# Kernel optimization log

Measured on AMD Instinct MI355X. Metric: run time of the kernel, lower is better.

Reference implementation:

```python
import jax, jax.numpy as jnp
import numpy as np

N = 100000
E = 800000
NFEAT = 128
NHID = 128
NCLASS = 40
THRESHOLD = 0.1
EPS = 1e-8


def setup_inputs() -> dict:
    key = jax.random.key(0)
    ks = jax.random.split(key, 12)
    x = jax.random.normal(ks[0], (N, NFEAT), dtype=jnp.float32)
    edge_index = jax.random.randint(ks[1], (2, E), 0, N, dtype=jnp.int64)
    edge_index2 = jax.random.randint(ks[2], (2, E), 0, N, dtype=jnp.int64)
    s1 = 1.0 / np.sqrt(NFEAT)
    s2 = 1.0 / np.sqrt(NHID)
    s3 = 1.0 / np.sqrt(NCLASS)
    W_gc1 = jax.random.uniform(ks[3], (NFEAT, NHID), jnp.float32, -s1, s1)
    b_gc1 = jax.random.uniform(ks[4], (NHID,), jnp.float32, -s1, s1)
    W_gc2 = jax.random.uniform(ks[5], (NHID, NCLASS), jnp.float32, -s2, s2)
    b_gc2 = jax.random.uniform(ks[6], (NCLASS,), jnp.float32, -s2, s2)
    W_att1 = jax.random.uniform(ks[7], (NCLASS, NCLASS), jnp.float32, -s3, s3)
    b_att1 = jax.random.uniform(ks[8], (NCLASS,), jnp.float32, -s3, s3)
    W_att2 = jax.random.uniform(ks[9], (NCLASS, 1), jnp.float32, -s3, s3)
    return {"x": x, "W_gc1": W_gc1, "b_gc1": b_gc1, "W_gc2": W_gc2,
            "b_gc2": b_gc2, "W_att1": W_att1, "b_att1": b_att1,
            "W_att2": W_att2, "edge_index": edge_index, "edge_index2": edge_index2}


def att_coef(feat, row, col, alive):
    # cosine similarity per edge; edges failing the threshold get weight 0
    # (exactly equivalent to removing them: contribute 0 to degree & messages).
    a = feat[row]          # [E, d]
    b = feat[col]          # [E, d]
    dot = jnp.sum(a * b, axis=-1)
    na = jnp.maximum(jnp.linalg.norm(a, axis=-1), EPS)
    nb = jnp.maximum(jnp.linalg.norm(b, axis=-1), EPS)
    sims = dot / (na * nb)
    mask = alive & (sims >= THRESHOLD)
    # original computes this under torch.no_grad()
    ew = jax.lax.stop_gradient(jnp.where(mask, sims, 0.0))
    return ew, mask


def gcn_conv(x, row, col, ew, W, b):
    # PyG GCNConv with add_self_loops=True, normalize=True on weighted adjacency
    h = x @ W                                     # [N, out]
    deg = jax.ops.segment_sum(ew, row, num_segments=N) + 1.0  # +1 self loop
    dinv = deg ** -0.5
    nw = dinv[row] * ew * dinv[col]               # [E]
    agg = jax.ops.segment_sum(h[col] * nw[:, None], row, num_segments=N)
    agg = agg + h * (dinv * dinv)[:, None]        # self-loop contribution
    return agg + b


def reference(x, W_gc1, b_gc1, W_gc2, b_gc2, W_att1, b_att1, W_att2,
              edge_index, edge_index2):
    r1, c1 = edge_index[0], edge_index[1]
    r2, c2 = edge_index2[0], edge_index2[1]
    ones = jnp.ones((E,), dtype=bool)

    ew2, m2 = att_coef(x, r2, c2, ones)
    ew1, m1 = att_coef(x, r1, c1, ones)

    x2 = jax.nn.relu(gcn_conv(x, r2, c2, ew2, W_gc1, b_gc1))
    x1 = jax.nn.relu(gcn_conv(x, r1, c1, ew1, W_gc1, b_gc1))
    # dropout is identity at eval time

    ew2b, _ = att_coef(x2, r2, c2, m2)
    ew1b, _ = att_coef(x1, r1, c1, m1)

    x2 = gcn_conv(x2, r2, c2, ew2b, W_gc2, b_gc2)
    x1 = gcn_conv(x1, r1, c1, ew1b, W_gc2, b_gc2)

    z = jnp.stack([x1, x2], axis=1)               # [N, 2, C]
    w = jnp.tanh(z @ W_att1 + b_att1) @ W_att2    # [N, 2, 1]
    beta = jax.nn.softmax(w, axis=1)
    fused = jnp.sum(beta * z, axis=1)             # [N, C]
    return jax.nn.log_softmax(fused, axis=1)
```

## Files before the change

### kernel.cpp

```cpp
#include <hip/hip_runtime.h>
#include <hip/hip_bf16.h>

#define NN 100000
#define EE 800000
#define THRV 0.1f
#define DELTA 0.008f
#define EPSV 1e-8f

#define ATOMIC_ADD_F32 unsafeAtomicAdd

__device__ inline int dot4(int a, int b, int c) {
#if __has_builtin(__builtin_amdgcn_sdot4)
    return __builtin_amdgcn_sdot4(a, b, c, false);
#else
    int s = c;
    #pragma unroll
    for (int k = 0; k < 4; k++) {
        int av = (a << (24 - 8 * k)) >> 24;
        int bv = (b << (24 - 8 * k)) >> 24;
        s += av * bv;
    }
    return s;
#endif
}


__global__ __launch_bounds__(256) void normalize_k(const float* __restrict__ x,
                                                   unsigned short* __restrict__ xq,
                                                   float* __restrict__ rs,
                                                   float* __restrict__ norms_x,
                                                   float* __restrict__ degL1) {
    int node = blockIdx.x * 4 + (threadIdx.x >> 6);
    int lane = threadIdx.x & 63;
    float2 v = reinterpret_cast<const float2*>(x)[(size_t)node * 64 + lane];
    float ss = v.x * v.x + v.y * v.y;
    float am = fmaxf(fabsf(v.x), fabsf(v.y));
    #pragma unroll
    for (int off = 32; off; off >>= 1) {
        ss += __shfl_xor(ss, off);
        am = fmaxf(am, __shfl_xor(am, off));
    }
    float norm = fmaxf(sqrtf(ss), EPSV);
    am = fmaxf(am, 1e-12f);
    float qs = 127.0f / am;
    int q0 = __float2int_rn(v.x * qs);
    int q1 = __float2int_rn(v.y * qs);
    unsigned short packed = (unsigned short)((q0 & 0xff) | ((q1 & 0xff) << 8));
    xq[(size_t)node * 64 + lane] = packed;
    if (lane == 0) {
        norms_x[node] = norm;
        rs[node] = am / (127.0f * norm);
        degL1[node] = 1.0f;
        degL1[node + NN] = 1.0f;
    }
}


__global__ __launch_bounds__(256) void edge_sim1_k(
        const unsigned short* __restrict__ xq, const float* __restrict__ rs,
        const float* __restrict__ x, const float* __restrict__ norms_x,
        const int* __restrict__ r1, const int* __restrict__ c1,
        const int* __restrict__ r2, const int* __restrict__ c2,
        float* __restrict__ ews, float* __restrict__ degL1,
        int* __restrict__ cnt) {
    int tid = threadIdx.x;
    int e = blockIdx.x * 16 + (tid >> 4);
    int l16 = tid & 15;
    int rnode, cnode, gr;
    if (e < EE) { rnode = r1[e]; cnode = c1[e]; gr = rnode; }
    else { int ee = e - EE; rnode = r2[ee]; cnode = c2[ee]; gr = NN + rnode; }
    int role = l16 >> 3;
    int j = l16 & 7;
    int node = role ? cnode : rnode;
    uint4 v = reinterpret_cast<const uint4*>(xq)[(size_t)node * 8 + j];
    uint4 p;
    p.x = (unsigned)__shfl_xor((int)v.x, 8);
    p.y = (unsigned)__shfl_xor((int)v.y, 8);
    p.z = (unsigned)__shfl_xor((int)v.z, 8);
    p.w = (unsigned)__shfl_xor((int)v.w, 8);
    int d = dot4((int)v.x, (int)p.x, 0);
    d = dot4((int)v.y, (int)p.y, d);
    d = dot4((int)v.z, (int)p.z, d);
    d = dot4((int)v.w, (int)p.w, d);
    #pragma unroll
    for (int off = 1; off < 8; off <<= 1) d += __shfl_xor(d, off);
    float sim = (float)d * rs[rnode] * rs[cnode];
    if (fabsf(sim - THRV) <= DELTA) {
        const float4* xa = reinterpret_cast<const float4*>(x + (size_t)rnode * 128);
        const float4* xb = reinterpret_cast<const float4*>(x + (size_t)cnode * 128);
        float df = 0.f;
        #pragma unroll
        for (int q = 0; q < 2; q++) {
            float4 a = xa[l16 + 16 * q];
            float4 b = xb[l16 + 16 * q];
            df += a.x * b.x + a.y * b.y + a.z * b.z + a.w * b.w;
        }
        #pragma unroll
        for (int off = 1; off < 16; off <<= 1) df += __shfl_xor(df, off);
        sim = df / (norms_x[rnode] * norms_x[cnode]);
    }
    float w = (sim >= THRV) ? sim : 0.0f;
    if (l16 == 0) {
        ews[e] = w;
        if (w != 0.0f) {
            ATOMIC_ADD_F32(&degL1[gr], w);
            atomicAdd(&cnt[gr], 1);
        }
    }
}


__global__ __launch_bounds__(512) void scan1_k(const int* __restrict__ in,
                                               int* __restrict__ out,
                                               int* __restrict__ partials, int n) {
    __shared__ int a[1024], b[1024];
    int t = threadIdx.x;
    int base = blockIdx.x * 1024;
    a[t]       = (base + t       < n) ? in[base + t]       : 0;
    a[t + 512] = (base + t + 512 < n) ? in[base + t + 512] : 0;
    __syncthreads();
    int* src = a; int* dst = b;
    for (int off = 1; off < 1024; off <<= 1) {
        #pragma unroll
        for (int q = 0; q < 2; q++) {
            int i = t + q * 512;
            int v = src[i];
            if (i >= off) v += src[i - off];
            dst[i] = v;
        }
        __syncthreads();
        int* tmp = src; src = dst; dst = tmp;
    }
    for (int q = 0; q < 2; q++) {
        int i = t + q * 512;
        if (base + i < n) out[base + i] = i ? src[i - 1] : 0;
    }
    if (t == 0) partials[blockIdx.x] = src[1023];
}

__global__ __launch_bounds__(256) void scan2_k(int* __restrict__ partials, int m) {
    __shared__ int a[256], b[256];
    int t = threadIdx.x;
    a[t] = (t < m) ? partials[t] : 0;
    __syncthreads();
    int* src = a; int* dst = b;
    for (int off = 1; off < 256; off <<= 1) {
        int v = src[t];
        if (t >= off) v += src[t - off];
        dst[t] = v;
        __syncthreads();
        int* tmp = src; src = dst; dst = tmp;
    }
    if (t < m) partials[t] = t ? src[t - 1] : 0;
}

__global__ void scan3_k(int* __restrict__ start, int* __restrict__ next,
                        const int* __restrict__ partials,
                        const int* __restrict__ cnt, int n) {
    int i = blockIdx.x * 256 + threadIdx.x;
    if (i < n) {
        int v = start[i] + partials[i >> 10];
        start[i] = v;
        next[i] = v;
        if (i == n - 1) start[n] = v + cnt[i];
    }
}


__global__ void scatter_alive_k(const int* __restrict__ r1, const int* __restrict__ c1,
                                const int* __restrict__ r2, const int* __restrict__ c2,
                                const float* __restrict__ ews,
                                const float* __restrict__ degL1,
                                int* __restrict__ next, int2* __restrict__ acw) {
    int e = blockIdx.x * 256 + threadIdx.x;
    float w = ews[e];
    if (w == 0.0f) return;
    int gr, c, sb;
    if (e < EE) { gr = r1[e]; c = c1[e]; sb = 0; }
    else        { gr = NN + r2[e - EE]; c = c2[e - EE]; sb = NN; }
    int pos = atomicAdd(&next[gr], 1);
    int2 rec;
    rec.x = c;
    rec.y = __float_as_int(w * rsqrtf(degL1[sb + c]));
    acw[pos] = rec;
}


__global__ __launch_bounds__(256) void gemm_nh_k(const float* __restrict__ A,
                                                 const float* __restrict__ W,
                                                 float* __restrict__ C, int n) {
    __shared__ float Ws[64 * 128];
    __shared__ float Xs[32 * 64];
    int tid = threadIdx.x;
    int row0 = blockIdx.x * 32;
    int cg = tid & 31;
    int rl = tid >> 5;
    float4 acc[4];
    #pragma unroll
    for (int i = 0; i < 4; i++) acc[i] = make_float4(0.f, 0.f, 0.f, 0.f);

    for (int kt = 0; kt < 2; kt++) {
        const float4* Wg = reinterpret_cast<const float4*>(W + kt * 64 * 128);
        float4* Ws4 = reinterpret_cast<float4*>(Ws);
        #pragma unroll
        for (int i = 0; i < 8; i++) Ws4[tid + 256 * i] = Wg[tid + 256 * i];
        float4* Xs4 = reinterpret_cast<float4*>(Xs);
        #pragma unroll
        for (int i = 0; i < 2; i++) {
            int idx = tid + 256 * i;
            int rr = idx >> 4, kq = idx & 15;
            int grow = row0 + rr; if (grow >= n) grow = n - 1;
            Xs4[idx] = reinterpret_cast<const float4*>(A + (size_t)grow * 128 + kt * 64)[kq];
        }
        __syncthreads();
        for (int k = 0; k < 64; k++) {
            float4 wv = reinterpret_cast<const float4*>(Ws + k * 128)[cg];
            #pragma unroll
            for (int r4 = 0; r4 < 4; r4++) {
                float xv = Xs[(rl + 8 * r4) * 64 + k];
                acc[r4].x += xv * wv.x; acc[r4].y += xv * wv.y;
                acc[r4].z += xv * wv.z; acc[r4].w += xv * wv.w;
            }
        }
        __syncthreads();
    }
    #pragma unroll
    for (int r4 = 0; r4 < 4; r4++) {
        int grow = row0 + rl + 8 * r4;
        if (grow < n) reinterpret_cast<float4*>(C + (size_t)grow * 128)[cg] = acc[r4];
    }
}


__global__ __launch_bounds__(256) void gemm_nc_k(const float* __restrict__ A,
                                                 const float* __restrict__ W,
                                                 float* __restrict__ C, int n) {
    __shared__ float Ws[128 * 40];
    __shared__ float Xs[64 * 130];
    int tid = threadIdx.x;
    int row0 = blockIdx.x * 64;
    for (int i = tid; i < 128 * 40; i += 256) Ws[i] = W[i];
    #pragma unroll
    for (int i = 0; i < 8; i++) {
        int idx = tid + 256 * i;
        int rr = idx >> 5, kq = idx & 31;
        int grow = row0 + rr; if (grow >= n) grow = n - 1;
        float4 v = reinterpret_cast<const float4*>(A + (size_t)grow * 128)[kq];
        float* dst = &Xs[rr * 130 + kq * 4];
        dst[0] = v.x; dst[1] = v.y; dst[2] = v.z; dst[3] = v.w;
    }
    __syncthreads();
    int c5 = tid & 7;
    int r  = tid >> 3;
    float acc0[5] = {0, 0, 0, 0, 0}, acc1[5] = {0, 0, 0, 0, 0};
    for (int k = 0; k < 128; k++) {
        float x0 = Xs[r * 130 + k], x1 = Xs[(r + 32) * 130 + k];
        #pragma unroll
        for (int c = 0; c < 5; c++) {
            float wv = Ws[k * 40 + c5 * 5 + c];
            acc0[c] += x0 * wv; acc1[c] += x1 * wv;
        }
    }
    int g0 = row0 + r, g1 = row0 + r + 32;
    if (g0 < n) {
        for (int c = 0; c < 5; c++) C[(size_t)g0 * 40 + c5 * 5 + c] = acc0[c];
    }
    if (g1 < n) {
        for (int c = 0; c < 5; c++) C[(size_t)g1 * 40 + c5 * 5 + c] = acc1[c];
    }
}


__global__ __launch_bounds__(256) void agg128_fused_k(
        const float* __restrict__ h, const int* __restrict__ start,
        const int2* __restrict__ acw, const float* __restrict__ degL1,
        const float* __restrict__ bias, float* __restrict__ agg,
        float* __restrict__ norms_l2, float* __restrict__ degL2) {
    int gr = blockIdx.x * 4 + (threadIdx.x >> 6);
    int lane = threadIdx.x & 63;
    int rnode = (gr < NN) ? gr : gr - NN;
    int j0 = start[gr], j1 = start[gr + 1];
    float2 acc = make_float2(0.f, 0.f);
    for (int j = j0; j < j1; j++) {
        int2 rec = acw[j];
        float wv = __int_as_float(rec.y);
        float2 hv = reinterpret_cast<const float2*>(h)[(size_t)rec.x * 64 + lane];
        acc.x += hv.x * wv;
        acc.y += hv.y * wv;
    }
    float dr = rsqrtf(degL1[gr]);
    float2 hs = reinterpret_cast<const float2*>(h)[(size_t)rnode * 64 + lane];
    float2 bb = reinterpret_cast<const float2*>(bias)[lane];
    float vx = fmaxf(acc.x * dr + hs.x * dr * dr + bb.x, 0.0f);
    float vy = fmaxf(acc.y * dr + hs.y * dr * dr + bb.y, 0.0f);
    reinterpret_cast<float2*>(agg)[(size_t)gr * 64 + lane] = make_float2(vx, vy);
    float ss = vx * vx + vy * vy;
    #pragma unroll
    for (int off = 32; off; off >>= 1) ss += __shfl_xor(ss, off);
    if (lane == 0) {
        norms_l2[gr] = fmaxf(sqrtf(ss), EPSV);
        degL2[gr] = 1.0f;
    }
}


__global__ __launch_bounds__(256) void edge_sim2_k(
        const float* __restrict__ agg, const float* __restrict__ norms_l2,
        const int* __restrict__ start, int2* __restrict__ acw,
        float* __restrict__ degL2) {
    int gr = blockIdx.x * 4 + (threadIdx.x >> 6);
    int lane = threadIdx.x & 63;
    int j0 = start[gr], j1 = start[gr + 1];
    if (j0 == j1) return;
    int set_base = (gr < NN) ? 0 : NN;
    float2 a = reinterpret_cast<const float2*>(agg)[(size_t)gr * 64 + lane];
    float nr = norms_l2[gr];
    float sum = 0.f;
    for (int j = j0; j < j1; j++) {
        int2 rec = acw[j];
        int cg = set_base + rec.x;
        float2 b = reinterpret_cast<const float2*>(agg)[(size_t)cg * 64 + lane];
        float d = a.x * b.x + a.y * b.y;
        #pragma unroll
        for (int off = 32; off; off >>= 1) d += __shfl_xor(d, off);
        float sim = d / (nr * norms_l2[cg]);
        float w2 = (sim >= THRV) ? sim : 0.0f;
        if (lane == 0) acw[j].y = __float_as_int(w2);
        sum += w2;
    }
    if (lane == 0) degL2[gr] = 1.0f + sum;
}


__global__ __launch_bounds__(256) void agg40_fused_k(
        const float* __restrict__ h2, const int* __restrict__ start,
        const int2* __restrict__ acw, const float* __restrict__ degL2,
        const float* __restrict__ bias, float* __restrict__ aggy) {
    int gr = blockIdx.x * 4 + (threadIdx.x >> 6);
    int lane = threadIdx.x & 63;
    int set_base = (gr < NN) ? 0 : NN;
    int j0 = start[gr], j1 = start[gr + 1];
    bool act = lane < 40;
    float acc = 0.f;
    for (int j = j0; j < j1; j++) {
        int2 rec = acw[j];
        float w2 = __int_as_float(rec.y);
        if (w2 == 0.0f) continue;
        int cg = set_base + rec.x;
        float nv = w2 * rsqrtf(degL2[cg]);
        if (act) acc += h2[(size_t)cg * 40 + lane] * nv;
    }
    if (act) {
        float dr = rsqrtf(degL2[gr]);
        float self = h2[(size_t)gr * 40 + lane];
        aggy[(size_t)gr * 40 + lane] = acc * dr + self * dr * dr + bias[lane];
    }
}


__global__ __launch_bounds__(256) void fusion_k(const float* __restrict__ y1,
                                                const float* __restrict__ y2,
                                                const float* __restrict__ W1,
                                                const float* __restrict__ b1,
                                                const float* __restrict__ W2,
                                                float* __restrict__ out, int n) {
    __shared__ float W1s[40 * 40];
    __shared__ float b1s[40];
    __shared__ float W2s[40];
    int tid = threadIdx.x;
    for (int i = tid; i < 1600; i += 256) W1s[i] = W1[i];
    if (tid < 40) { b1s[tid] = b1[tid]; W2s[tid] = W2[tid]; }
    __syncthreads();
    int i = blockIdx.x * 256 + tid;
    if (i >= n) return;
    float z1[40], z2[40];
    const float4* y14 = reinterpret_cast<const float4*>(y1 + (size_t)i * 40);
    const float4* y24 = reinterpret_cast<const float4*>(y2 + (size_t)i * 40);
    #pragma unroll
    for (int q = 0; q < 10; q++) {
        float4 a = y14[q], b = y24[q];
        z1[4 * q] = a.x; z1[4 * q + 1] = a.y; z1[4 * q + 2] = a.z; z1[4 * q + 3] = a.w;
        z2[4 * q] = b.x; z2[4 * q + 1] = b.y; z2[4 * q + 2] = b.z; z2[4 * q + 3] = b.w;
    }
    float w1 = 0.f, w2 = 0.f;
    for (int c = 0; c < 40; c++) {
        float s1 = b1s[c], s2 = b1s[c];
        for (int j = 0; j < 40; j++) {
            float ww = W1s[j * 40 + c];
            s1 += z1[j] * ww; s2 += z2[j] * ww;
        }
        float wa = W2s[c];
        w1 += tanhf(s1) * wa; w2 += tanhf(s2) * wa;
    }
    float m = fmaxf(w1, w2);
    float e1 = expf(w1 - m), e2 = expf(w2 - m);
    float inv = 1.0f / (e1 + e2);
    float be1 = e1 * inv, be2 = e2 * inv;
    float fu[40];
    float mx = -1e30f;
    #pragma unroll
    for (int c = 0; c < 40; c++) {
        fu[c] = be1 * z1[c] + be2 * z2[c];
        mx = fmaxf(mx, fu[c]);
    }
    float se = 0.f;
    #pragma unroll
    for (int c = 0; c < 40; c++) se += expf(fu[c] - mx);
    float ls = logf(se);
    float4* o4 = reinterpret_cast<float4*>(out + (size_t)i * 40);
    #pragma unroll
    for (int q = 0; q < 10; q++) {
        float4 v;
        v.x = fu[4 * q] - mx - ls; v.y = fu[4 * q + 1] - mx - ls;
        v.z = fu[4 * q + 2] - mx - ls; v.w = fu[4 * q + 3] - mx - ls;
        o4[q] = v;
    }
}


extern "C" void kernel_launch(void* const* d_in, const int* in_sizes, int n_in,
                              void* d_out, int out_size, void* d_ws, size_t ws_size,
                              hipStream_t stream) {
    (void)in_sizes; (void)n_in; (void)out_size; (void)ws_size;
    const float* x   = (const float*)d_in[0];
    const float* Wg1 = (const float*)d_in[1];
    const float* bg1 = (const float*)d_in[2];
    const float* Wg2 = (const float*)d_in[3];
    const float* bg2 = (const float*)d_in[4];
    const float* Wa1 = (const float*)d_in[5];
    const float* ba1 = (const float*)d_in[6];
    const float* Wa2 = (const float*)d_in[7];
    const int* ei1 = (const int*)d_in[8];
    const int* ei2 = (const int*)d_in[9];
    const int *r1 = ei1, *c1 = ei1 + EE;
    const int *r2 = ei2, *c2 = ei2 + EE;
    float* out = (float*)d_out;

    float* ws = (float*)d_ws;
    float* norms_x  = ws;  ws += NN;
    float* norms_l2 = ws;  ws += 2 * NN;
    float* rs       = ws;  ws += NN;
    float* degL1    = ws;  ws += 2 * NN;
    float* degL2    = ws;  ws += 2 * NN;
    int*   cnt      = (int*)ws;  ws += 2 * NN;
    int*   start    = (int*)ws;  ws += 2 * NN + 8;
    int*   next     = (int*)ws;  ws += 2 * NN;
    int*   partials = (int*)ws;  ws += 512;
    float* ews      = ws;  ws += 2 * EE;
    int2*  acw      = (int2*)ws; ws += (size_t)2 * 2 * EE;
    float* h        = ws;  ws += (size_t)NN * 128;
    float* agg      = ws;  ws += (size_t)2 * NN * 128;
    unsigned short* xq = (unsigned short*)agg;
    float* h2   = h;
    float* aggy = agg;

    const int twoN = 2 * NN;
    const int twoE = 2 * EE;
    const int scan_blocks = (twoN + 1023) / 1024;

    (void)hipMemsetAsync(cnt, 0, sizeof(int) * twoN, stream);
    normalize_k<<<NN / 4, 256, 0, stream>>>(x, xq, rs, norms_x, degL1);
    edge_sim1_k<<<twoE / 16, 256, 0, stream>>>(xq, rs, x, norms_x,
                                               r1, c1, r2, c2, ews, degL1, cnt);

    scan1_k<<<scan_blocks, 512, 0, stream>>>(cnt, start, partials, twoN);
    scan2_k<<<1, 256, 0, stream>>>(partials, scan_blocks);
    scan3_k<<<(twoN + 255) / 256, 256, 0, stream>>>(start, next, partials, cnt, twoN);
    scatter_alive_k<<<twoE / 256, 256, 0, stream>>>(r1, c1, r2, c2, ews, degL1,
                                                    next, acw);

    gemm_nh_k<<<NN / 32, 256, 0, stream>>>(x, Wg1, h, NN);
    agg128_fused_k<<<twoN / 4, 256, 0, stream>>>(h, start, acw, degL1, bg1,
                                                 agg, norms_l2, degL2);

    edge_sim2_k<<<twoN / 4, 256, 0, stream>>>(agg, norms_l2, start, acw, degL2);
    gemm_nc_k<<<twoN / 64, 256, 0, stream>>>(agg, Wg2, h2, twoN);
    agg40_fused_k<<<twoN / 4, 256, 0, stream>>>(h2, start, acw, degL2, bg2, aggy);

    fusion_k<<<(NN + 255) / 256, 256, 0, stream>>>(aggy, aggy + (size_t)NN * 40,
                                                   Wa1, ba1, Wa2, out, NN);
}
```

Baseline: 472.7 us.

## Quantize layer-1 activations to int8 for second-layer edge similarity screening

The first-layer aggregation kernel now also writes an int8-quantized copy of each activation row plus a per-row scale. A new second-layer edge-similarity kernel reads these 2-byte-per-lane values instead of fp32 rows, and falls back to exact fp32 only when the approximate similarity lies near the threshold. The goal is less gather bandwidth per edge. Separately, the first edge-similarity kernel now handles each edge with 8 lanes instead of 16, each lane doing two 16-byte loads, so there are fewer shuffles and more edges per block. The quantized path is only taken when the workspace is large enough, and it relies on the DELTA band to keep thresholding exact.

```diff
diff --git a/kernel.cpp b/kernel.cpp
--- a/kernel.cpp
+++ b/kernel.cpp
@@ -64,43 +64,54 @@
         float* __restrict__ ews, float* __restrict__ degL1,
         int* __restrict__ cnt) {
     int tid = threadIdx.x;
-    int e = blockIdx.x * 16 + (tid >> 4);
-    int l16 = tid & 15;
+    int e = blockIdx.x * 32 + (tid >> 3);
+    int q = tid & 7;
     int rnode, cnode, gr;
     if (e < EE) { rnode = r1[e]; cnode = c1[e]; gr = rnode; }
     else { int ee = e - EE; rnode = r2[ee]; cnode = c2[ee]; gr = NN + rnode; }
-    int role = l16 >> 3;
-    int j = l16 & 7;
+    int role = q >> 2;
+    int j = q & 3;
     int node = role ? cnode : rnode;
-    uint4 v = reinterpret_cast<const uint4*>(xq)[(size_t)node * 8 + j];
-    uint4 p;
-    p.x = (unsigned)__shfl_xor((int)v.x, 8);
-    p.y = (unsigned)__shfl_xor((int)v.y, 8);
-    p.z = (unsigned)__shfl_xor((int)v.z, 8);
-    p.w = (unsigned)__shfl_xor((int)v.w, 8);
-    int d = dot4((int)v.x, (int)p.x, 0);
-    d = dot4((int)v.y, (int)p.y, d);
-    d = dot4((int)v.z, (int)p.z, d);
-    d = dot4((int)v.w, (int)p.w, d);
-    #pragma unroll
-    for (int off = 1; off < 8; off <<= 1) d += __shfl_xor(d, off);
+    const uint4* base = reinterpret_cast<const uint4*>(xq) + (size_t)node * 8 + j * 2;
+    uint4 v0 = base[0];
+    uint4 v1 = base[1];
+    uint4 p0, p1;
+    p0.x = (unsigned)__shfl_xor((int)v0.x, 4);
+    p0.y = (unsigned)__shfl_xor((int)v0.y, 4);
+    p0.z = (unsigned)__shfl_xor((int)v0.z, 4);
+    p0.w = (unsigned)__shfl_xor((int)v0.w, 4);
+    p1.x = (unsigned)__shfl_xor((int)v1.x, 4);
+    p1.y = (unsigned)__shfl_xor((int)v1.y, 4);
+    p1.z = (unsigned)__shfl_xor((int)v1.z, 4);
+    p1.w = (unsigned)__shfl_xor((int)v1.w, 4);
+    int d = dot4((int)v0.x, (int)p0.x, 0);
+    d = dot4((int)v0.y, (int)p0.y, d);
+    d = dot4((int)v0.z, (int)p0.z, d);
+    d = dot4((int)v0.w, (int)p0.w, d);
+    d = dot4((int)v1.x, (int)p1.x, d);
+    d = dot4((int)v1.y, (int)p1.y, d);
+    d = dot4((int)v1.z, (int)p1.z, d);
+    d = dot4((int)v1.w, (int)p1.w, d);
+    d += __shfl_xor(d, 1);
+    d += __shfl_xor(d, 2);
     float sim = (float)d * rs[rnode] * rs[cnode];
     if (fabsf(sim - THRV) <= DELTA) {
         const float4* xa = reinterpret_cast<const float4*>(x + (size_t)rnode * 128);
         const float4* xb = reinterpret_cast<const float4*>(x + (size_t)cnode * 128);
         float df = 0.f;
         #pragma unroll
-        for (int q = 0; q < 2; q++) {
-            float4 a = xa[l16 + 16 * q];
-            float4 b = xb[l16 + 16 * q];
+        for (int t = 0; t < 4; t++) {
+            float4 a = xa[q + 8 * t];
+            float4 b = xb[q + 8 * t];
             df += a.x * b.x + a.y * b.y + a.z * b.z + a.w * b.w;
         }
-        #pragma unroll
-        for (int off = 1; off < 16; off <<= 1) df += __shfl_xor(df, off);
+        df += __shfl_xor(df, 1);
+        df += __shfl_xor(df, 2);
+        df += __shfl_xor(df, 4);
         sim = df / (norms_x[rnode] * norms_x[cnode]);
     }
     float w = (sim >= THRV) ? sim : 0.0f;
-    if (l16 == 0) {
+    if (q == 0) {
         ews[e] = w;
         if (w != 0.0f) {
             ATOMIC_ADD_F32(&degL1[gr], w);
@@ -271,11 +282,13 @@
 }
 
 
+template<int WQ>
 __global__ __launch_bounds__(256) void agg128_fused_k(
         const float* __restrict__ h, const int* __restrict__ start,
         const int2* __restrict__ acw, const float* __restrict__ degL1,
         const float* __restrict__ bias, float* __restrict__ agg,
-        float* __restrict__ norms_l2, float* __restrict__ degL2) {
+        float* __restrict__ norms_l2, float* __restrict__ degL2,
+        unsigned short* __restrict__ xq2, float* __restrict__ rs2) {
     int gr = blockIdx.x * 4 + (threadIdx.x >> 6);
     int lane = threadIdx.x & 63;
     int rnode = (gr < NN) ? gr : gr - NN;
@@ -295,10 +308,24 @@
     float vy = fmaxf(acc.y * dr + hs.y * dr * dr + bb.y, 0.0f);
     reinterpret_cast<float2*>(agg)[(size_t)gr * 64 + lane] = make_float2(vx, vy);
     float ss = vx * vx + vy * vy;
-    #pragma unroll
-    for (int off = 32; off; off >>= 1) ss += __shfl_xor(ss, off);
+    float am = fmaxf(vx, vy);
+    #pragma unroll
+    for (int off = 32; off; off >>= 1) {
+        ss += __shfl_xor(ss, off);
+        am = fmaxf(am, __shfl_xor(am, off));
+    }
+    float norm = fmaxf(sqrtf(ss), EPSV);
+    if (WQ) {
+        am = fmaxf(am, 1e-12f);
+        float qs = 127.0f / am;
+        int q0 = __float2int_rn(vx * qs);
+        int q1 = __float2int_rn(vy * qs);
+        xq2[(size_t)gr * 64 + lane] =
+            (unsigned short)((q0 & 0xff) | ((q1 & 0xff) << 8));
+        if (lane == 0) rs2[gr] = am / (127.0f * norm);
+    }
     if (lane == 0) {
-        norms_l2[gr] = fmaxf(sqrtf(ss), EPSV);
+        norms_l2[gr] = norm;
         degL2[gr] = 1.0f;
     }
 }
@@ -324,6 +351,48 @@
         #pragma unroll
         for (int off = 32; off; off >>= 1) d += __shfl_xor(d, off);
         float sim = d / (nr * norms_l2[cg]);
+        float w2 = (sim >= THRV) ? sim : 0.0f;
+        if (lane == 0) acw[j].y = __float_as_int(w2);
+        sum += w2;
+    }
+    if (lane == 0) degL2[gr] = 1.0f + sum;
+}
+
+
+__global__ __launch_bounds__(256) void edge_sim2_q_k(
+        const unsigned short* __restrict__ xq2, const float* __restrict__ rs2,
+        const float* __restrict__ agg, const float* __restrict__ norms_l2,
+        const int* __restrict__ start, int2* __restrict__ acw,
+        float* __restrict__ degL2) {
+    int gr = blockIdx.x * 4 + (threadIdx.x >> 6);
+    int lane = threadIdx.x & 63;
+    int j0 = start[gr], j1 = start[gr + 1];
+    if (j0 == j1) return;
+    int set_base = (gr < NN) ? 0 : NN;
+    unsigned int au = xq2[(size_t)gr * 64 + lane];
+    int a0 = ((int)(au << 24)) >> 24;
+    int a1 = ((int)(au << 16)) >> 24;
+    float ra = rs2[gr];
+    float nr = norms_l2[gr];
+    float sum = 0.f;
+    for (int j = j0; j < j1; j++) {
+        int2 rec = acw[j];
+        int cg = set_base + rec.x;
+        unsigned int bu = xq2[(size_t)cg * 64 + lane];
+        int b0 = ((int)(bu << 24)) >> 24;
+        int b1 = ((int)(bu << 16)) >> 24;
+        int d = a0 * b0 + a1 * b1;
+        #pragma unroll
+        for (int off = 32; off; off >>= 1) d += __shfl_xor(d, off);
+        float sim = (float)d * ra * rs2[cg];
+        if (fabsf(sim - THRV) <= DELTA) {
+            float2 a = reinterpret_cast<const float2*>(agg)[(size_t)gr * 64 + lane];
+            float2 b = reinterpret_cast<const float2*>(agg)[(size_t)cg * 64 + lane];
+            float df = a.x * b.x + a.y * b.y;
+            #pragma unroll
+            for (int off = 32; off; off >>= 1) df += __shfl_xor(df, off);
+            sim = df / (nr * norms_l2[cg]);
+        }
         float w2 = (sim >= THRV) ? sim : 0.0f;
         if (lane == 0) acw[j].y = __float_as_int(w2);
         sum += w2;
@@ -421,7 +490,7 @@
 extern "C" void kernel_launch(void* const* d_in, const int* in_sizes, int n_in,
                               void* d_out, int out_size, void* d_ws, size_t ws_size,
                               hipStream_t stream) {
-    (void)in_sizes; (void)n_in; (void)out_size; (void)ws_size;
+    (void)in_sizes; (void)n_in; (void)out_size;
     const float* x   = (const float*)d_in[0];
     const float* Wg1 = (const float*)d_in[1];
     const float* bg1 = (const float*)d_in[2];
@@ -436,20 +505,26 @@
     const int *r2 = ei2, *c2 = ei2 + EE;
     float* out = (float*)d_out;
 
-    float* ws = (float*)d_ws;
-    float* norms_x  = ws;  ws += NN;
-    float* norms_l2 = ws;  ws += 2 * NN;
-    float* rs       = ws;  ws += NN;
-    float* degL1    = ws;  ws += 2 * NN;
-    float* degL2    = ws;  ws += 2 * NN;
-    int*   cnt      = (int*)ws;  ws += 2 * NN;
-    int*   start    = (int*)ws;  ws += 2 * NN + 8;
-    int*   next     = (int*)ws;  ws += 2 * NN;
-    int*   partials = (int*)ws;  ws += 512;
-    float* ews      = ws;  ws += 2 * EE;
-    int2*  acw      = (int2*)ws; ws += (size_t)2 * 2 * EE;
-    float* h        = ws;  ws += (size_t)NN * 128;
-    float* agg      = ws;  ws += (size_t)2 * NN * 128;
+    float* wp = (float*)d_ws;
+    float* norms_x  = wp;  wp += NN;
+    float* norms_l2 = wp;  wp += 2 * NN;
+    float* rs       = wp;  wp += NN;
+    float* degL1    = wp;  wp += 2 * NN;
+    float* degL2    = wp;  wp += 2 * NN;
+    int*   cnt      = (int*)wp;  wp += 2 * NN;
+    int*   start    = (int*)wp;  wp += 2 * NN + 8;
+    int*   next     = (int*)wp;  wp += 2 * NN;
+    int*   partials = (int*)wp;  wp += 512;
+    float* ews      = wp;  wp += 2 * EE;
+    int2*  acw      = (int2*)wp; wp += (size_t)2 * 2 * EE;
+    float* h        = wp;  wp += (size_t)NN * 128;
+    float* agg      = wp;  wp += (size_t)2 * NN * 128;
+    float* rs2            = wp;
+    unsigned short* xq2   = (unsigned short*)(wp + 2 * NN);
+    size_t bytes_q = ((size_t)(wp - (float*)d_ws) + 2 * NN + (size_t)2 * NN * 32)
+                     * sizeof(float);
+    bool useq = ws_size >= bytes_q;
+
     unsigned short* xq = (unsigned short*)agg;
     float* h2   = h;
     float* aggy = agg;
@@ -460,7 +535,7 @@
 
     (void)hipMemsetAsync(cnt, 0, sizeof(int) * twoN, stream);
     normalize_k<<<NN / 4, 256, 0, stream>>>(x, xq, rs, norms_x, degL1);
-    edge_sim1_k<<<twoE / 16, 256, 0, stream>>>(xq, rs, x, norms_x,
+    edge_sim1_k<<<twoE / 32, 256, 0, stream>>>(xq, rs, x, norms_x,
                                                r1, c1, r2, c2, ews, degL1, cnt);
 
     scan1_k<<<scan_blocks, 512, 0, stream>>>(cnt, start, partials, twoN);
@@ -470,10 +545,21 @@
                                                     next, acw);
 
     gemm_nh_k<<<NN / 32, 256, 0, stream>>>(x, Wg1, h, NN);
-    agg128_fused_k<<<twoN / 4, 256, 0, stream>>>(h, start, acw, degL1, bg1,
-                                                 agg, norms_l2, degL2);
-
-    edge_sim2_k<<<twoN / 4, 256, 0, stream>>>(agg, norms_l2, start, acw, degL2);
+    if (useq) {
+        agg128_fused_k<1><<<twoN / 4, 256, 0, stream>>>(h, start, acw, degL1, bg1,
+                                                        agg, norms_l2, degL2, xq2, rs2);
+    } else {
+        agg128_fused_k<0><<<twoN / 4, 256, 0, stream>>>(h, start, acw, degL1, bg1,
+                                                        agg, norms_l2, degL2,
+                                                        nullptr, nullptr);
+    }
+
+    if (useq) {
+        edge_sim2_q_k<<<twoN / 4, 256, 0, stream>>>(xq2, rs2, agg, norms_l2,
+                                                    start, acw, degL2);
+    } else {
+        edge_sim2_k<<<twoN / 4, 256, 0, stream>>>(agg, norms_l2, start, acw, degL2);
+    }
     gemm_nc_k<<<twoN / 64, 256, 0, stream>>>(agg, Wg2, h2, twoN);
     agg40_fused_k<<<twoN / 4, 256, 0, stream>>>(h2, start, acw, degL2, bg2, aggy);
 
```

After: 468.5 us. Within noise of the previous version (-0.9%).
